# Kernel optimization log

Measured on AMD Instinct MI355X. Metric: run time of the kernel, lower is better.

The kernel has to match this reference:

```python
import jax, jax.numpy as jnp
import numpy as np

B, S, H = 32, 1024, 512  # batch, src_len, hidden_dim


def setup_inputs() -> dict:
    key = jax.random.key(0)
    k1, k2, k3, k4, k5 = jax.random.split(key, 5)
    hidden = jax.random.normal(k1, (B, H), dtype=jnp.float32)
    encoder_outputs = jax.random.normal(k2, (B, S, 2 * H), dtype=jnp.float32)
    # nn.Linear(3H, H): weight stored here as [3H, H] (input-major) with bias [H]
    W = jax.random.normal(k3, (3 * H, H), dtype=jnp.float32) / np.sqrt(3 * H)
    b = jax.random.normal(k4, (H,), dtype=jnp.float32) * 0.01
    v = jax.random.normal(k5, (H,), dtype=jnp.float32) / np.sqrt(H)
    return {"hidden": hidden, "encoder_outputs": encoder_outputs, "W": W, "b": b, "v": v}


def reference(hidden, encoder_outputs, W, b, v):
    # concat((repeat(hidden), encoder_outputs)) @ W  ==  hidden @ W[:H] (broadcast) + enc @ W[H:]
    Wh, We = W[:H], W[H:]                         # [H,H], [2H,H]
    h_proj = hidden @ Wh                           # [B,H]
    e_proj = jnp.einsum('bse,eh->bsh', encoder_outputs, We)  # [B,S,H]
    energy = jnp.tanh(h_proj[:, None, :] + e_proj + b)       # [B,S,H]
    # bmm(v[B,1,H], energy^T[B,H,S]) -> scores [B,S]
    scores = jnp.einsum('bsh,h->bs', energy, v)
    return jax.nn.softmax(scores, axis=1)
```

## Files before the change

kernel.cpp:

```cpp
#include <hip/hip_runtime.h>
#include <math.h>

#define B_ 32
#define S_ 1024
#define H_ 512
#define K_ 1024
#define M_ (B_ * S_)

typedef __attribute__((ext_vector_type(8))) short bf16x8;
typedef __attribute__((ext_vector_type(4))) float f32x4;

__device__ __forceinline__ void split_bf16(float f, unsigned short& hi, unsigned short& lo) {
    unsigned u = __float_as_uint(f);
    unsigned rh = (u + 0x7fffu + ((u >> 16) & 1u)) >> 16;
    hi = (unsigned short)rh;
    float fh = __uint_as_float(rh << 16);
    float r = f - fh;
    unsigned ur = __float_as_uint(r);
    unsigned rl = (ur + 0x7fffu + ((ur >> 16) & 1u)) >> 16;
    lo = (unsigned short)rl;
}

__device__ __forceinline__ void async_copy16(const void* g, void* l) {
    __builtin_amdgcn_global_load_lds(
        (const __attribute__((address_space(1))) void*)g,
        (__attribute__((address_space(3))) void*)l, 16, 0, 0);
}

__global__ __launch_bounds__(256) void split_eo_kernel(
    const float* __restrict__ EO, unsigned short* __restrict__ EOh,
    unsigned short* __restrict__ EOl)
{
    const size_t i = ((size_t)blockIdx.x * 256 + threadIdx.x) * 8;
    const float4 a = *reinterpret_cast<const float4*>(EO + i);
    const float4 b = *reinterpret_cast<const float4*>(EO + i + 4);
    union { unsigned short us[8]; uint4 u4; } h, l;
    split_bf16(a.x, h.us[0], l.us[0]);
    split_bf16(a.y, h.us[1], l.us[1]);
    split_bf16(a.z, h.us[2], l.us[2]);
    split_bf16(a.w, h.us[3], l.us[3]);
    split_bf16(b.x, h.us[4], l.us[4]);
    split_bf16(b.y, h.us[5], l.us[5]);
    split_bf16(b.z, h.us[6], l.us[6]);
    split_bf16(b.w, h.us[7], l.us[7]);
    *reinterpret_cast<uint4*>(EOh + i) = h.u4;
    *reinterpret_cast<uint4*>(EOl + i) = l.u4;
}

__global__ __launch_bounds__(256) void hproj_kernel(
    const float* __restrict__ hidden, const float* __restrict__ W,
    const float* __restrict__ bias, float* __restrict__ hb)
{
    const int tid = threadIdx.x;
    const int h0  = blockIdx.x * 64;
    const int b   = blockIdx.y;
    const int h   = h0 + (tid & 63);
    const int ks  = tid >> 6;
    const float* hrow = hidden + b * H_;
    float acc = 0.f;
    #pragma unroll 8
    for (int k = ks * 128; k < ks * 128 + 128; ++k)
        acc = fmaf(hrow[k], W[(size_t)k * H_ + h], acc);
    __shared__ float red[4][64];
    red[ks][tid & 63] = acc;
    __syncthreads();
    if (tid < 64)
        hb[b * H_ + h0 + tid] = red[0][tid] + red[1][tid] + red[2][tid] + red[3][tid]
                              + bias[h0 + tid];
}

__global__ __launch_bounds__(256) void conv_we_kernel(
    const float* __restrict__ We, unsigned short* __restrict__ Wh,
    unsigned short* __restrict__ Wl)
{
    __shared__ float t[32][33];
    const int tx = threadIdx.x & 31, ty = threadIdx.x >> 5;
    const int k0 = blockIdx.x * 32, n0 = blockIdx.y * 32;
    #pragma unroll
    for (int j = 0; j < 4; ++j) {
        const int k = ty + 8 * j;
        t[k][tx] = We[(size_t)(k0 + k) * H_ + n0 + tx];
    }
    __syncthreads();
    #pragma unroll
    for (int j = 0; j < 4; ++j) {
        const int n = ty + 8 * j;
        unsigned short hi, lo;
        split_bf16(t[tx][n], hi, lo);
        Wh[(size_t)(n0 + n) * K_ + k0 + tx] = hi;
        Wl[(size_t)(n0 + n) * K_ + k0 + tx] = lo;
    }
}

__global__ __launch_bounds__(256, 3) void gemm_mfma_pre(
    const unsigned short* __restrict__ EOh, const unsigned short* __restrict__ EOl,
    const unsigned short* __restrict__ Bth, const unsigned short* __restrict__ Btl,
    const float* __restrict__ hb, const float* __restrict__ v,
    float* __restrict__ partial)
{
    __shared__ unsigned short lds[4 * 128 * 32];
    unsigned short* Ah = lds;
    unsigned short* Al = lds + 4096;
    unsigned short* Bh = lds + 8192;
    unsigned short* Bl = lds + 12288;

    const int tid  = threadIdx.x;
    const int nt   = blockIdx.x;
    const int mt   = blockIdx.y;
    const int row0 = mt * 128;
    const int col0 = nt * 128;
    const int batch = row0 >> 10;

    const int lane   = tid & 63;
    const int wave   = tid >> 6;
    const int wm     = wave >> 1, wn = wave & 1;
    const int lanelo = lane & 15, quad = lane >> 4;

    const int rl = lane >> 2;
    const int qs = lane & 3;

    size_t ga[2], gb[2];
    int ldsoff[2];
    #pragma unroll
    for (int j = 0; j < 2; ++j) {
        const int iss = wave * 2 + j;
        const int r   = iss * 16 + rl;
        const int qg  = qs ^ ((r >> 1) & 3);
        ga[j] = (size_t)(row0 + r) * K_ + qg * 8;
        gb[j] = (size_t)(col0 + r) * K_ + qg * 8;
        ldsoff[j] = iss * 512;
    }

    f32x4 acc[4][4];
    #pragma unroll
    for (int i = 0; i < 4; ++i)
        #pragma unroll
        for (int j = 0; j < 4; ++j)
            acc[i][j] = (f32x4){0.f, 0.f, 0.f, 0.f};

    for (int k0 = 0; k0 < K_; k0 += 32) {
        #pragma unroll
        for (int j = 0; j < 2; ++j) {
            async_copy16(EOh + ga[j] + k0, Ah + ldsoff[j]);
            async_copy16(EOl + ga[j] + k0, Al + ldsoff[j]);
            async_copy16(Bth + gb[j] + k0, Bh + ldsoff[j]);
            async_copy16(Btl + gb[j] + k0, Bl + ldsoff[j]);
        }
        __syncthreads();

        bf16x8 a_h[4], a_l[4], b_h[4], b_l[4];
        #pragma unroll
        for (int fi = 0; fi < 4; ++fi) {
            const int m  = wm * 64 + fi * 16 + lanelo;
            const int sa = quad ^ ((m >> 1) & 3);
            a_h[fi] = *reinterpret_cast<const bf16x8*>(&Ah[m * 32 + sa * 8]);
            a_l[fi] = *reinterpret_cast<const bf16x8*>(&Al[m * 32 + sa * 8]);
            const int n  = wn * 64 + fi * 16 + lanelo;
            const int sb = quad ^ ((n >> 1) & 3);
            b_h[fi] = *reinterpret_cast<const bf16x8*>(&Bh[n * 32 + sb * 8]);
            b_l[fi] = *reinterpret_cast<const bf16x8*>(&Bl[n * 32 + sb * 8]);
        }
        #pragma unroll
        for (int fi = 0; fi < 4; ++fi)
            #pragma unroll
            for (int fj = 0; fj < 4; ++fj) {
                acc[fi][fj] = __builtin_amdgcn_mfma_f32_16x16x32_bf16(
                    a_h[fi], b_h[fj], acc[fi][fj], 0, 0, 0);
                acc[fi][fj] = __builtin_amdgcn_mfma_f32_16x16x32_bf16(
                    a_h[fi], b_l[fj], acc[fi][fj], 0, 0, 0);
                acc[fi][fj] = __builtin_amdgcn_mfma_f32_16x16x32_bf16(
                    a_l[fi], b_h[fj], acc[fi][fj], 0, 0, 0);
            }
        __syncthreads();
    }

    const float* hb_row = hb + batch * H_;
    float hbv[4], vv[4];
    #pragma unroll
    for (int fj = 0; fj < 4; ++fj) {
        const int c = col0 + wn * 64 + fj * 16 + lanelo;
        hbv[fj] = hb_row[c];
        vv[fj]  = v[c];
    }
    float* red = reinterpret_cast<float*>(lds);
    #pragma unroll
    for (int fi = 0; fi < 4; ++fi)
        #pragma unroll
        for (int r = 0; r < 4; ++r) {
            float rs = 0.f;
            #pragma unroll
            for (int fj = 0; fj < 4; ++fj)
                rs = fmaf(tanhf(acc[fi][fj][r] + hbv[fj]), vv[fj], rs);
            rs += __shfl_xor(rs, 1, 64);
            rs += __shfl_xor(rs, 2, 64);
            rs += __shfl_xor(rs, 4, 64);
            rs += __shfl_xor(rs, 8, 64);
            if (lanelo == 0) {
                const int row = wm * 64 + fi * 16 + quad * 4 + r;
                red[row * 2 + wn] = rs;
            }
        }
    __syncthreads();
    if (tid < 128)
        partial[(size_t)nt * M_ + row0 + tid] = red[tid * 2] + red[tid * 2 + 1];
}

#define AST 40
__global__ __launch_bounds__(256, 3) void fused_attn_gemm_mfma(
    const float* __restrict__ EO, const unsigned short* __restrict__ Bth,
    const unsigned short* __restrict__ Btl, const float* __restrict__ hb,
    const float* __restrict__ v, float* __restrict__ partial)
{
    __shared__ unsigned short Ah[128 * AST];
    __shared__ unsigned short Al[128 * AST];
    __shared__ unsigned short Bh[128 * AST];
    __shared__ unsigned short Bl[128 * AST];
    const int tid  = threadIdx.x;
    const int nt   = blockIdx.x;
    const int mt   = blockIdx.y;
    const int row0 = mt * 128, col0 = nt * 128;
    const int batch = row0 >> 10;
    const int lane = tid & 63, wave = tid >> 6;
    const int wm = wave >> 1, wn = wave & 1;
    const int lanelo = lane & 15, quad = lane >> 4;
    f32x4 acc[4][4];
    #pragma unroll
    for (int i = 0; i < 4; ++i)
        #pragma unroll
        for (int j = 0; j < 4; ++j) acc[i][j] = (f32x4){0.f, 0.f, 0.f, 0.f};
    for (int k0 = 0; k0 < K_; k0 += 32) {
        #pragma unroll
        for (int q = 0; q < 4; ++q) {
            const int f = tid + 256 * q;
            const int m = f >> 3, c = f & 7;
            const float4 av = *reinterpret_cast<const float4*>(
                EO + (size_t)(row0 + m) * K_ + k0 + c * 4);
            union { unsigned short us[4]; uint2 u2; } ph, pl;
            split_bf16(av.x, ph.us[0], pl.us[0]);
            split_bf16(av.y, ph.us[1], pl.us[1]);
            split_bf16(av.z, ph.us[2], pl.us[2]);
            split_bf16(av.w, ph.us[3], pl.us[3]);
            *reinterpret_cast<uint2*>(&Ah[m * AST + c * 4]) = ph.u2;
            *reinterpret_cast<uint2*>(&Al[m * AST + c * 4]) = pl.u2;
        }
        #pragma unroll
        for (int q = 0; q < 2; ++q) {
            const int s = tid + 256 * q;
            const int n = s >> 2, qq = s & 3;
            const size_t g = (size_t)(col0 + n) * K_ + k0 + qq * 8;
            *reinterpret_cast<uint4*>(&Bh[n * AST + qq * 8]) =
                *reinterpret_cast<const uint4*>(Bth + g);
            *reinterpret_cast<uint4*>(&Bl[n * AST + qq * 8]) =
                *reinterpret_cast<const uint4*>(Btl + g);
        }
        __syncthreads();
        bf16x8 a_h[4], a_l[4], b_h[4], b_l[4];
        #pragma unroll
        for (int fi = 0; fi < 4; ++fi) {
            const int m = wm * 64 + fi * 16 + lanelo;
            a_h[fi] = *reinterpret_cast<const bf16x8*>(&Ah[m * AST + quad * 8]);
            a_l[fi] = *reinterpret_cast<const bf16x8*>(&Al[m * AST + quad * 8]);
            const int n = wn * 64 + fi * 16 + lanelo;
            b_h[fi] = *reinterpret_cast<const bf16x8*>(&Bh[n * AST + quad * 8]);
            b_l[fi] = *reinterpret_cast<const bf16x8*>(&Bl[n * AST + quad * 8]);
        }
        #pragma unroll
        for (int fi = 0; fi < 4; ++fi)
            #pragma unroll
            for (int fj = 0; fj < 4; ++fj) {
                acc[fi][fj] = __builtin_amdgcn_mfma_f32_16x16x32_bf16(
                    a_h[fi], b_h[fj], acc[fi][fj], 0, 0, 0);
                acc[fi][fj] = __builtin_amdgcn_mfma_f32_16x16x32_bf16(
                    a_h[fi], b_l[fj], acc[fi][fj], 0, 0, 0);
                acc[fi][fj] = __builtin_amdgcn_mfma_f32_16x16x32_bf16(
                    a_l[fi], b_h[fj], acc[fi][fj], 0, 0, 0);
            }
        __syncthreads();
    }
    const float* hb_row = hb + batch * H_;
    float hbv[4], vv[4];
    #pragma unroll
    for (int fj = 0; fj < 4; ++fj) {
        const int c = col0 + wn * 64 + fj * 16 + lanelo;
        hbv[fj] = hb_row[c];
        vv[fj]  = v[c];
    }
    float* red = reinterpret_cast<float*>(Ah);
    #pragma unroll
    for (int fi = 0; fi < 4; ++fi)
        #pragma unroll
        for (int r = 0; r < 4; ++r) {
            float rs = 0.f;
            #pragma unroll
            for (int fj = 0; fj < 4; ++fj)
                rs = fmaf(tanhf(acc[fi][fj][r] + hbv[fj]), vv[fj], rs);
            rs += __shfl_xor(rs, 1, 64);
            rs += __shfl_xor(rs, 2, 64);
            rs += __shfl_xor(rs, 4, 64);
            rs += __shfl_xor(rs, 8, 64);
            if (lanelo == 0) {
                const int row = wm * 64 + fi * 16 + quad * 4 + r;
                red[row * 2 + wn] = rs;
            }
        }
    __syncthreads();
    if (tid < 128)
        partial[(size_t)nt * M_ + row0 + tid] = red[tid * 2] + red[tid * 2 + 1];
}

__global__ __launch_bounds__(256) void softmax_kernel(
    const float* __restrict__ partial, float* __restrict__ out)
{
    const int b = blockIdx.x;
    const int tid = threadIdx.x;
    float val[4];
    float lmax = -3.0e38f;
    #pragma unroll
    for (int q = 0; q < 4; ++q) {
        const int idx = b * S_ + tid + 256 * q;
        float sum = partial[idx] + partial[M_ + idx] + partial[2 * M_ + idx] +
                    partial[3 * M_ + idx];
        val[q] = sum;
        lmax = fmaxf(lmax, sum);
    }
    #pragma unroll
    for (int off = 32; off > 0; off >>= 1)
        lmax = fmaxf(lmax, __shfl_down(lmax, off, 64));
    __shared__ float wmax[4];
    if ((tid & 63) == 0) wmax[tid >> 6] = lmax;
    __syncthreads();
    const float gmax = fmaxf(fmaxf(wmax[0], wmax[1]), fmaxf(wmax[2], wmax[3]));
    float lsum = 0.0f;
    #pragma unroll
    for (int q = 0; q < 4; ++q) {
        val[q] = expf(val[q] - gmax);
        lsum += val[q];
    }
    #pragma unroll
    for (int off = 32; off > 0; off >>= 1)
        lsum += __shfl_down(lsum, off, 64);
    __shared__ float wsum[4];
    if ((tid & 63) == 0) wsum[tid >> 6] = lsum;
    __syncthreads();
    const float inv = 1.0f / (wsum[0] + wsum[1] + wsum[2] + wsum[3]);
    #pragma unroll
    for (int q = 0; q < 4; ++q)
        out[b * S_ + tid + 256 * q] = val[q] * inv;
}

extern "C" void kernel_launch(void* const* d_in, const int* in_sizes, int n_in,
                              void* d_out, int out_size, void* d_ws, size_t ws_size,
                              hipStream_t stream) {
    const float* hidden = (const float*)d_in[0];
    const float* EO     = (const float*)d_in[1];
    const float* W      = (const float*)d_in[2];
    const float* bias   = (const float*)d_in[3];
    const float* v      = (const float*)d_in[4];
    float* out          = (float*)d_out;

    float* hb      = (float*)d_ws;
    float* partial = hb + B_ * H_;
    unsigned short* Wth = (unsigned short*)(partial + 4 * M_);
    unsigned short* Wtl = Wth + (size_t)H_ * K_;
    unsigned short* EOh = Wtl + (size_t)H_ * K_;
    unsigned short* EOl = EOh + (size_t)M_ * K_;

    const size_t need_small = (size_t)(B_ * H_ + 4 * M_) * sizeof(float)
                            + (size_t)H_ * K_ * 2 * sizeof(unsigned short);
    const size_t need_full  = need_small
                            + (size_t)M_ * K_ * 2 * sizeof(unsigned short);

    const float* We = W + (size_t)H_ * H_;

    hproj_kernel<<<dim3(8, B_), 256, 0, stream>>>(hidden, W, bias, hb);
    conv_we_kernel<<<dim3(K_ / 32, H_ / 32), 256, 0, stream>>>(We, Wth, Wtl);
    if (ws_size >= need_full) {
        split_eo_kernel<<<(size_t)M_ * K_ / (256 * 8), 256, 0, stream>>>(EO, EOh, EOl);
        gemm_mfma_pre<<<dim3(4, M_ / 128), 256, 0, stream>>>(EOh, EOl, Wth, Wtl, hb, v, partial);
    } else {
        fused_attn_gemm_mfma<<<dim3(4, M_ / 128), 256, 0, stream>>>(EO, Wth, Wtl, hb, v, partial);
    }
    softmax_kernel<<<B_, 256, 0, stream>>>(partial, out);
}
```

Measured before the change: 354.6 us.

## Double-buffer LDS tiles in split-bf16 GEMM and retile the split kernel

Result: faster. 347.0 us (-2.1%).

```diff
diff --git a/kernel.cpp b/kernel.cpp
--- a/kernel.cpp
+++ b/kernel.cpp
@@ -31,20 +31,21 @@
     const float* __restrict__ EO, unsigned short* __restrict__ EOh,
     unsigned short* __restrict__ EOl)
 {
-    const size_t i = ((size_t)blockIdx.x * 256 + threadIdx.x) * 8;
-    const float4 a = *reinterpret_cast<const float4*>(EO + i);
-    const float4 b = *reinterpret_cast<const float4*>(EO + i + 4);
-    union { unsigned short us[8]; uint4 u4; } h, l;
-    split_bf16(a.x, h.us[0], l.us[0]);
-    split_bf16(a.y, h.us[1], l.us[1]);
-    split_bf16(a.z, h.us[2], l.us[2]);
-    split_bf16(a.w, h.us[3], l.us[3]);
-    split_bf16(b.x, h.us[4], l.us[4]);
-    split_bf16(b.y, h.us[5], l.us[5]);
-    split_bf16(b.z, h.us[6], l.us[6]);
-    split_bf16(b.w, h.us[7], l.us[7]);
-    *reinterpret_cast<uint4*>(EOh + i) = h.u4;
-    *reinterpret_cast<uint4*>(EOl + i) = l.u4;
+    const size_t base = (size_t)blockIdx.x * 4096 + (size_t)threadIdx.x * 4;
+    float4 a[4];
+    #pragma unroll
+    for (int j = 0; j < 4; ++j)
+        a[j] = *reinterpret_cast<const float4*>(EO + base + j * 1024);
+    #pragma unroll
+    for (int j = 0; j < 4; ++j) {
+        union { unsigned short us[4]; uint2 u2; } h, l;
+        split_bf16(a[j].x, h.us[0], l.us[0]);
+        split_bf16(a[j].y, h.us[1], l.us[1]);
+        split_bf16(a[j].z, h.us[2], l.us[2]);
+        split_bf16(a[j].w, h.us[3], l.us[3]);
+        *reinterpret_cast<uint2*>(EOh + base + j * 1024) = h.u2;
+        *reinterpret_cast<uint2*>(EOl + base + j * 1024) = l.u2;
+    }
 }
 
 __global__ __launch_bounds__(256) void hproj_kernel(
@@ -92,17 +93,13 @@
     }
 }
 
-__global__ __launch_bounds__(256, 3) void gemm_mfma_pre(
+__global__ __launch_bounds__(256, 2) void gemm_mfma_pre(
     const unsigned short* __restrict__ EOh, const unsigned short* __restrict__ EOl,
     const unsigned short* __restrict__ Bth, const unsigned short* __restrict__ Btl,
     const float* __restrict__ hb, const float* __restrict__ v,
     float* __restrict__ partial)
 {
-    __shared__ unsigned short lds[4 * 128 * 32];
-    unsigned short* Ah = lds;
-    unsigned short* Al = lds + 4096;
-    unsigned short* Bh = lds + 8192;
-    unsigned short* Bl = lds + 12288;
+    __shared__ unsigned short lds[2][4][4096];
 
     const int tid  = threadIdx.x;
     const int nt   = blockIdx.x;
@@ -138,27 +135,40 @@
         for (int j = 0; j < 4; ++j)
             acc[i][j] = (f32x4){0.f, 0.f, 0.f, 0.f};
 
-    for (int k0 = 0; k0 < K_; k0 += 32) {
-        #pragma unroll
-        for (int j = 0; j < 2; ++j) {
-            async_copy16(EOh + ga[j] + k0, Ah + ldsoff[j]);
-            async_copy16(EOl + ga[j] + k0, Al + ldsoff[j]);
-            async_copy16(Bth + gb[j] + k0, Bh + ldsoff[j]);
-            async_copy16(Btl + gb[j] + k0, Bl + ldsoff[j]);
-        }
+    #pragma unroll
+    for (int j = 0; j < 2; ++j) {
+        async_copy16(EOh + ga[j], &lds[0][0][ldsoff[j]]);
+        async_copy16(EOl + ga[j], &lds[0][1][ldsoff[j]]);
+        async_copy16(Bth + gb[j], &lds[0][2][ldsoff[j]]);
+        async_copy16(Btl + gb[j], &lds[0][3][ldsoff[j]]);
+    }
+
+    for (int i = 0; i < 32; ++i) {
         __syncthreads();
+        const int cur = i & 1;
+        if (i < 31) {
+            const int nxt = (i + 1) & 1;
+            const int k0 = 32 * (i + 1);
+            #pragma unroll
+            for (int j = 0; j < 2; ++j) {
+                async_copy16(EOh + ga[j] + k0, &lds[nxt][0][ldsoff[j]]);
+                async_copy16(EOl + ga[j] + k0, &lds[nxt][1][ldsoff[j]]);
+                async_copy16(Bth + gb[j] + k0, &lds[nxt][2][ldsoff[j]]);
+                async_copy16(Btl + gb[j] + k0, &lds[nxt][3][ldsoff[j]]);
+            }
+        }
 
         bf16x8 a_h[4], a_l[4], b_h[4], b_l[4];
         #pragma unroll
         for (int fi = 0; fi < 4; ++fi) {
             const int m  = wm * 64 + fi * 16 + lanelo;
             const int sa = quad ^ ((m >> 1) & 3);
-            a_h[fi] = *reinterpret_cast<const bf16x8*>(&Ah[m * 32 + sa * 8]);
-            a_l[fi] = *reinterpret_cast<const bf16x8*>(&Al[m * 32 + sa * 8]);
+            a_h[fi] = *reinterpret_cast<const bf16x8*>(&lds[cur][0][m * 32 + sa * 8]);
+            a_l[fi] = *reinterpret_cast<const bf16x8*>(&lds[cur][1][m * 32 + sa * 8]);
             const int n  = wn * 64 + fi * 16 + lanelo;
             const int sb = quad ^ ((n >> 1) & 3);
-            b_h[fi] = *reinterpret_cast<const bf16x8*>(&Bh[n * 32 + sb * 8]);
-            b_l[fi] = *reinterpret_cast<const bf16x8*>(&Bl[n * 32 + sb * 8]);
+            b_h[fi] = *reinterpret_cast<const bf16x8*>(&lds[cur][2][n * 32 + sb * 8]);
+            b_l[fi] = *reinterpret_cast<const bf16x8*>(&lds[cur][3][n * 32 + sb * 8]);
         }
         #pragma unroll
         for (int fi = 0; fi < 4; ++fi)
@@ -171,7 +181,6 @@
                 acc[fi][fj] = __builtin_amdgcn_mfma_f32_16x16x32_bf16(
                     a_l[fi], b_h[fj], acc[fi][fj], 0, 0, 0);
             }
-        __syncthreads();
     }
 
     const float* hb_row = hb + batch * H_;
@@ -182,7 +191,7 @@
         hbv[fj] = hb_row[c];
         vv[fj]  = v[c];
     }
-    float* red = reinterpret_cast<float*>(lds);
+    float* red = reinterpret_cast<float*>(&lds[0][0][0]);
     #pragma unroll
     for (int fi = 0; fi < 4; ++fi)
         #pragma unroll
@@ -375,7 +384,7 @@
     hproj_kernel<<<dim3(8, B_), 256, 0, stream>>>(hidden, W, bias, hb);
     conv_we_kernel<<<dim3(K_ / 32, H_ / 32), 256, 0, stream>>>(We, Wth, Wtl);
     if (ws_size >= need_full) {
-        split_eo_kernel<<<(size_t)M_ * K_ / (256 * 8), 256, 0, stream>>>(EO, EOh, EOl);
+        split_eo_kernel<<<(size_t)M_ * K_ / 4096, 256, 0, stream>>>(EO, EOh, EOl);
         gemm_mfma_pre<<<dim3(4, M_ / 128), 256, 0, stream>>>(EOh, EOl, Wth, Wtl, hb, v, partial);
     } else {
         fused_attn_gemm_mfma<<<dim3(4, M_ / 128), 256, 0, stream>>>(EO, Wth, Wtl, hb, v, partial);
```
